# Performance work log

Hardware: AMD Instinct MI355X
Metric: run time of the kernel (lower is better)

The kernel has to match this reference:

```python
import jax, jax.numpy as jnp
import numpy as np

N_IN, N_LAT, LEN_T, N_SHIFT = 128, 21, 51, 50
N_HID, BATCH = 4, 2048


def identity_init(n_rows, n_cols):
    A = np.zeros((n_rows, n_cols), np.float32)
    if n_rows >= n_cols:
        k = n_rows - n_cols + 1
        for c in range(n_cols):
            A[c:c + k, c] = 1.0 / k
    else:
        k = n_cols - n_rows + 1
        for r in range(n_rows):
            A[r, r:r + k] = 1.0 / k
    return jnp.asarray(A)


def setup_inputs() -> dict:
    key = jax.random.key(0)
    ks = jax.random.split(key, 8)
    s = 0.05
    return {
        'inputs': jax.random.normal(ks[0], (BATCH, LEN_T, N_IN), dtype=jnp.float32),
        'enc_W': jax.random.normal(ks[1], (N_HID, N_IN, N_IN), dtype=jnp.float32) * s,
        'enc_b': jnp.zeros((N_HID, N_IN), jnp.float32),
        'enc_Wout': jax.random.normal(ks[2], (N_IN, N_IN), dtype=jnp.float32) * s,
        'enc_bout': jnp.zeros((N_IN,), jnp.float32),
        'dec_W': jax.random.normal(ks[3], (N_HID, N_IN, N_IN), dtype=jnp.float32) * s,
        'dec_b': jnp.zeros((N_HID, N_IN), jnp.float32),
        'dec_Wout': jax.random.normal(ks[4], (N_IN, N_IN), dtype=jnp.float32) * s,
        'dec_bout': jnp.zeros((N_IN,), jnp.float32),
        'W_enc_inner': identity_init(N_IN, N_LAT),
        'L': jnp.eye(N_LAT, dtype=jnp.float32),
        'W_dec_inner': identity_init(N_LAT, N_IN),
    }


def res_block(x, Ws, bs, Wout, bout):
    # DenseResBlock: ReLU hidden dense stack + linear output + identity skip
    h = x
    for i in range(Ws.shape[0]):
        h = jax.nn.relu(h @ Ws[i] + bs[i])
    return h @ Wout + bout + x


def reference(inputs, enc_W, enc_b, enc_Wout, enc_bout,
              dec_W, dec_b, dec_Wout, dec_bout,
              W_enc_inner, L, W_dec_inner):
    B = inputs.shape[0]
    len_pred = LEN_T - N_SHIFT  # = 1

    # ---- autoencoder branch (all timesteps flattened into rows) ----
    auto_in = inputs.reshape(-1, N_IN)                       # [B*T, n_in]
    part_enc = res_block(auto_in, enc_W, enc_b, enc_Wout, enc_bout)
    full_enc = part_enc @ W_enc_inner                        # [B*T, n_lat]
    part_dec = full_enc @ W_dec_inner                        # [B*T, n_in]
    autoencoder_output = res_block(part_dec, dec_W, dec_b, dec_Wout, dec_bout)
    autoencoder_output = autoencoder_output.reshape(B, LEN_T, N_IN)
    outer_auto_output = res_block(part_enc, dec_W, dec_b, dec_Wout, dec_bout)
    outer_auto_output = outer_auto_output.reshape(B, LEN_T, N_IN)

    # ---- prediction branch: recurrent application of Koopman operator L ----
    pred_in = inputs[:, :len_pred, :].reshape(-1, N_IN)      # [B*len_pred, n_in]
    cur = res_block(pred_in, enc_W, enc_b, enc_Wout, enc_bout) @ W_enc_inner

    def step(cur_enc, _):
        adv = cur_enc @ L                                    # [B*len_pred, n_lat]
        dec = res_block(adv @ W_dec_inner, dec_W, dec_b, dec_Wout, dec_bout)
        return adv, dec

    _, preds = jax.lax.scan(step, cur, None, length=N_SHIFT)  # [S, B*lp, n_in]
    preds = preds.reshape(N_SHIFT, B, len_pred, N_IN)
    predictions = preds.transpose(1, 0, 2, 3).reshape(B, N_SHIFT * len_pred, N_IN)

    return autoencoder_output, outer_auto_output, predictions
```

## Files before the change

kernel.cpp:

```cpp
#include <hip/hip_runtime.h>
#include <stdint.h>


typedef _Float16 h8 __attribute__((ext_vector_type(8)));
typedef _Float16 h4 __attribute__((ext_vector_type(4)));
typedef float    f4 __attribute__((ext_vector_type(4)));

#define ROWS_AUTO 104448
#define NT64      1632
#define NUNITS    1952

#define WT_ENCW      0
#define WT_ENCWOUT   (4*16384)
#define WT_DECW      (5*16384)
#define WT_DECWOUT   (9*16384)
#define WT_COMB      (10*16384)

#define MFULL_OFF_B 0x60000
#define ACH_OFF_B   0x200000
#define PE_OFF_B    0x220000
#define PET0_OFF_B  0x1C00000

#define H0 0
#define H1 16384
#define H2 32768
#define H3 49152
#define LDSE 51712
#define LDSD 68096

#define hsw(rl, c) ((rl)*256 + ((((c)) ^ ((rl) & 7)) << 4))

#define PIN(B) asm volatile("" : "+v"(B[0]), "+v"(B[1]), "+v"(B[2]), "+v"(B[3]), \
                                 "+v"(B[4]), "+v"(B[5]), "+v"(B[6]), "+v"(B[7]))

__device__ __forceinline__ f4 mfma16(h8 a, h8 b, f4 c) {
  return __builtin_amdgcn_mfma_f32_16x16x32_f16(a, b, c, 0, 0, 0);
}
__device__ __forceinline__ h8 cvt8(f4 a, f4 b) {
  h8 r;
  r[0]=(_Float16)a[0]; r[1]=(_Float16)a[1]; r[2]=(_Float16)a[2]; r[3]=(_Float16)a[3];
  r[4]=(_Float16)b[0]; r[5]=(_Float16)b[1]; r[6]=(_Float16)b[2]; r[7]=(_Float16)b[3];
  return r;
}
__device__ __forceinline__ void loadW(h8 B[8], const _Float16* gW, int nbase, int r15, int hi) {
#pragma unroll
  for (int nt = 0; nt < 2; ++nt)
#pragma unroll
    for (int ks = 0; ks < 4; ++ks)
      B[nt*4+ks] = *(const h8*)(gW + (size_t)(nbase + nt*16 + r15)*128 + ks*32 + hi*8);
}

__device__ __forceinline__ void mmF4s(const char* sm, int hb, const h8 B[8],
                                      f4 acc[4][2], int r15, int hi) {
#pragma unroll
  for (int rt = 0; rt < 4; ++rt) { acc[rt][0] = (f4){0,0,0,0}; acc[rt][1] = (f4){0,0,0,0}; }
#pragma unroll
  for (int ks = 0; ks < 4; ++ks) {
    int c = ks*4 + hi;
    h8 a[4];
#pragma unroll
    for (int rt = 0; rt < 4; ++rt) a[rt] = *(const h8*)(sm + hb + hsw(rt*16 + r15, c));
#pragma unroll
    for (int rt = 0; rt < 4; ++rt) {
      acc[rt][0] = mfma16(B[ks],   a[rt], acc[rt][0]);
      acc[rt][1] = mfma16(B[4+ks], a[rt], acc[rt][1]);
    }
  }
}

__device__ __forceinline__ void hw4s(char* sm, int hb, int wbase, const f4 acc[4][2],
                                     const float* bl, int bo, int r15, int hi) {
  f4 bb0 = *(const f4*)(bl + bo + wbase + hi*4);
  f4 bb1 = *(const f4*)(bl + bo + wbase + 16 + hi*4);
  int bo2 = (hi & 1) * 8;
#pragma unroll
  for (int nt = 0; nt < 2; ++nt) {
    int c = ((wbase + nt*16) >> 3) + (hi >> 1);
    f4 bb = nt ? bb1 : bb0;
#pragma unroll
    for (int rt = 0; rt < 4; ++rt) {
      int row = rt*16 + r15;
      h4 p;
#pragma unroll
      for (int d = 0; d < 4; ++d) p[d] = (_Float16)fmaxf(acc[rt][nt][d] + bb[d], 0.f);
      *(h4*)(sm + hb + row*256 + ((c ^ (row & 7)) << 4) + bo2) = p;
    }
  }
}
__device__ __forceinline__ void hw4r(char* sm, int hb, int wbase, const f4 acc[4][2],
                                     int r15, int hi) {
  int bo2 = (hi & 1) * 8;
#pragma unroll
  for (int nt = 0; nt < 2; ++nt) {
    int c = ((wbase + nt*16) >> 3) + (hi >> 1);
#pragma unroll
    for (int rt = 0; rt < 4; ++rt) {
      int row = rt*16 + r15;
      h4 p;
#pragma unroll
      for (int d = 0; d < 4; ++d) p[d] = (_Float16)acc[rt][nt][d];
      *(h4*)(sm + hb + row*256 + ((c ^ (row & 7)) << 4) + bo2) = p;
    }
  }
}

__device__ __forceinline__ void epi_store(char* sm, int hskip, int htr, int wbase,
                                          const f4 acc[4][2], const float* bl,
                                          float* dst, int rstride,
                                          int tid, int r15, int hi) {
  f4 bb0 = *(const f4*)(bl + 512 + wbase + hi*4);
  f4 bb1 = *(const f4*)(bl + 512 + wbase + 16 + hi*4);
  int bo2 = (hi & 1) * 8;
#pragma unroll
  for (int nt = 0; nt < 2; ++nt) {
    int c = ((wbase + nt*16) >> 3) + (hi >> 1);
    int q = (wbase >> 2) + nt*4 + hi;
    f4 bb = nt ? bb1 : bb0;
#pragma unroll
    for (int rt = 0; rt < 4; ++rt) {
      int row = rt*16 + r15;
      h4 sk = *(const h4*)(sm + hskip + row*256 + ((c ^ (row & 7)) << 4) + bo2);
      f4 v;
#pragma unroll
      for (int d = 0; d < 4; ++d) v[d] = acc[rt][nt][d] + bb[d] + (float)sk[d];
      *(f4*)(sm + htr + row*512 + ((q ^ ((row & 7) << 2)) << 4)) = v;
    }
  }
  __syncthreads();
#pragma unroll
  for (int i = 0; i < 8; ++i) {
    int idx = i*256 + tid, row = idx >> 5, q = idx & 31;
    f4 v = *(const f4*)(sm + htr + row*512 + ((q ^ ((row & 7) << 2)) << 4));
    *(f4*)(dst + (size_t)row*rstride + q*4) = v;
  }
}

#define LAYD(HIN, HOUT, BW, BO) do {                                 \
    mmF4s(sm, HIN, BW, acc, r15, hi);                                \
    hw4s(sm, HOUT, wbase, acc, bl, BO, r15, hi);                     \
    __syncthreads();                                                 \
  } while (0)


__global__ __launch_bounds__(512) void k_prep(
    const float* __restrict__ encW, const float* __restrict__ encWout,
    const float* __restrict__ decW, const float* __restrict__ decWout,
    const float* __restrict__ L,
    _Float16* __restrict__ wt, float* __restrict__ ach) {
  __shared__ float chA[441], chB[441];
  int m = blockIdx.y, tid = threadIdx.x;
  if (m == 10) {
    if (blockIdx.x != 0) return;
    if (tid < 441) chA[tid] = L[tid];
    __syncthreads();
    for (int s = 0; s < 50; ++s) {
      if (tid < 441) ach[s*441 + tid] = chA[tid];
      if (s == 49) break;
      if (tid < 441) {
        int i = tid / 21, j = tid % 21; float a = 0.f;
        for (int k = 0; k < 21; ++k) a += chA[i*21 + k] * L[k*21 + j];
        chB[tid] = a;
      }
      __syncthreads();
      if (tid < 441) chA[tid] = chB[tid];
      __syncthreads();
    }
    return;
  }
  int idx = blockIdx.x*512 + tid;
  if (idx >= 16384) return;
  const float* src; _Float16* dst;
  if (m < 4)       { src = encW + m*16384;     dst = wt + WT_ENCW + m*16384; }
  else if (m == 4) { src = encWout;            dst = wt + WT_ENCWOUT; }
  else if (m < 9)  { src = decW + (m-5)*16384; dst = wt + WT_DECW + (m-5)*16384; }
  else             { src = decWout;            dst = wt + WT_DECWOUT; }
  int n = idx >> 7, k = idx & 127;
  dst[idx] = (_Float16)src[k*128 + n];
}

__global__ __launch_bounds__(512) void k_aux(
    const float* __restrict__ ach, const float* __restrict__ wencI,
    const float* __restrict__ wdecI,
    _Float16* __restrict__ mfull, _Float16* __restrict__ wt) {
  __shared__ float T1[2688];
  __shared__ float sa[441];
  int s = blockIdx.x, t = threadIdx.x;
  if (s < 50) {
    if (t < 441) sa[t] = ach[s*441 + t];
    __syncthreads();
    for (int idx = t; idx < 2688; idx += 512) {
      int k = idx / 21, j = idx % 21;
      float a = 0.f;
      for (int u = 0; u < 21; ++u) a += wencI[k*21 + u] * sa[u*21 + j];
      T1[idx] = a;
    }
  } else {
    for (int idx = t; idx < 2688; idx += 512) T1[idx] = wencI[idx];
  }
  __syncthreads();
  _Float16* dst = (s < 50) ? (mfull + (size_t)s*16384) : (wt + WT_COMB);
  for (int idx = t; idx < 16384; idx += 512) {
    int n = idx >> 7, k = idx & 127;
    float a = 0.f;
    for (int j = 0; j < 21; ++j) a += T1[k*21 + j] * wdecI[j*128 + n];
    dst[idx] = (_Float16)a;
  }
}


__global__ __launch_bounds__(256, 2) void k_enc(
    const float* __restrict__ x, const _Float16* __restrict__ wt,
    const float* __restrict__ enc_b, const float* __restrict__ enc_bout,
    _Float16* __restrict__ pe_ws, _Float16* __restrict__ pet0) {
  __shared__ char sm[LDSE];
  float* bl = (float*)(sm + 49152);
  int tid = threadIdx.x, lane = tid & 63;
  int r15 = lane & 15, hi = lane >> 4;
  int wbase = (tid >> 6) * 32;
  h8 B0[8], B1[8], B2[8], B3[8], B4[8];
  loadW(B0, wt + WT_ENCW,           wbase, r15, hi);
  loadW(B1, wt + WT_ENCW + 16384,   wbase, r15, hi);
  loadW(B2, wt + WT_ENCW + 2*16384, wbase, r15, hi);
  loadW(B3, wt + WT_ENCW + 3*16384, wbase, r15, hi);
  loadW(B4, wt + WT_ENCWOUT,        wbase, r15, hi);
  PIN(B0); PIN(B1); PIN(B2); PIN(B3); PIN(B4);
  bl[tid] = enc_b[tid]; bl[256 + tid] = enc_b[256 + tid];
  if (tid < 128) bl[512 + tid] = enc_bout[tid];
  f4 acc[4][2];

  for (int t = blockIdx.x; t < NT64; t += gridDim.x) {
    size_t rb = (size_t)t * 64;
#pragma unroll
    for (int i = 0; i < 4; ++i) {
      int idx = i*256 + tid, rl = idx >> 4, c = idx & 15;
      const float* s = x + (rb + rl)*128 + c*8;
      f4 v0 = *(const f4*)s, v1 = *(const f4*)(s + 4);
      *(h8*)(sm + H0 + hsw(rl, c)) = cvt8(v0, v1);
    }
    __syncthreads();
    LAYD(H0, H1, B0, 0); LAYD(H1, H2, B1, 128);
    LAYD(H2, H1, B2, 256); LAYD(H1, H2, B3, 384);
    mmF4s(sm, H2, B4, acc, r15, hi);
    {
      f4 bb0 = *(const f4*)(bl + 512 + wbase + hi*4);
      f4 bb1 = *(const f4*)(bl + 512 + wbase + 16 + hi*4);
      int bo2 = (hi & 1) * 8;
#pragma unroll
      for (int nt = 0; nt < 2; ++nt) {
        int c = ((wbase + nt*16) >> 3) + (hi >> 1);
        f4 bb = nt ? bb1 : bb0;
#pragma unroll
        for (int rt = 0; rt < 4; ++rt) {
          int row = rt*16 + r15;
          int soff = row*256 + ((c ^ (row & 7)) << 4) + bo2;
          h4 sk = *(const h4*)(sm + H0 + soff);
          h4 p;
#pragma unroll
          for (int d = 0; d < 4; ++d) p[d] = (_Float16)(acc[rt][nt][d] + bb[d] + (float)sk[d]);
          *(h4*)(sm + H1 + soff) = p;
        }
      }
    }
    __syncthreads();
    {
      char* g = (char*)(pe_ws) + (size_t)t*16384;
#pragma unroll
      for (int i = 0; i < 4; ++i) {
        int idx = i*256 + tid, off = idx*16;
        f4 v = *(const f4*)(sm + H1 + off);
        *(f4*)(g + off) = v;
        int rl = idx >> 4, slot = idx & 15;
        size_t rg = rb + (size_t)rl;
        if (rg % 51u == 0u) {
          int c = slot ^ (rl & 7);
          *(f4*)((char*)pet0 + (rg/51u)*256 + c*16) = v;
        }
      }
    }
  }
}


__global__ __launch_bounds__(256, 2) void k_decpred(
    const _Float16* __restrict__ wt, const _Float16* __restrict__ pe_ws,
    const _Float16* __restrict__ pet0, const _Float16* __restrict__ mfull,
    const float* __restrict__ dec_b, const float* __restrict__ dec_bout,
    float* __restrict__ out1, float* __restrict__ out2, float* __restrict__ out3) {
  __shared__ char sm[LDSD];
  float* bl = (float*)(sm + 65536);
  int tid = threadIdx.x, lane = tid & 63;
  int r15 = lane & 15, hi = lane >> 4;
  int wbase = (tid >> 6) * 32;
  h8 B0[8], B1[8], B2[8], B3[8], B4[8];
  loadW(B0, wt + WT_DECW,           wbase, r15, hi);
  loadW(B1, wt + WT_DECW + 16384,   wbase, r15, hi);
  loadW(B2, wt + WT_DECW + 2*16384, wbase, r15, hi);
  loadW(B3, wt + WT_DECW + 3*16384, wbase, r15, hi);
  loadW(B4, wt + WT_DECWOUT,        wbase, r15, hi);
  PIN(B0); PIN(B1); PIN(B2); PIN(B3); PIN(B4);
  bl[tid] = dec_b[tid]; bl[256 + tid] = dec_b[256 + tid];
  if (tid < 128) bl[512 + tid] = dec_bout[tid];
  f4 acc[4][2];

  for (int u = blockIdx.x; u < NUNITS; u += gridDim.x) {
    __syncthreads();
    if (u < NT64) {
      const char* src = (const char*)pe_ws + (size_t)u*16384;
      float* d2 = out2 + (size_t)u*64*128;
      float* d1 = out1 + (size_t)u*64*128;
#pragma unroll
      for (int i = 0; i < 4; ++i) {
        int off = (i*256 + tid)*16;
        *(f4*)(sm + H0 + off) = *(const f4*)(src + off);
      }
      __syncthreads();
      LAYD(H0, H1, B0, 0); LAYD(H1, H2, B1, 128);
      LAYD(H2, H1, B2, 256); LAYD(H1, H2, B3, 384);
      mmF4s(sm, H2, B4, acc, r15, hi);
      __syncthreads();
      epi_store(sm, H0, H1, wbase, acc, bl, d2, 128, tid, r15, hi);
      {
        h8 Bc[8];
        loadW(Bc, wt + WT_COMB, wbase, r15, hi);
        mmF4s(sm, H0, Bc, acc, r15, hi);
      }
      hw4r(sm, H3, wbase, acc, r15, hi);
      __syncthreads();
      LAYD(H3, H0, B0, 0); LAYD(H0, H1, B1, 128);
      LAYD(H1, H0, B2, 256); LAYD(H0, H1, B3, 384);
      mmF4s(sm, H1, B4, acc, r15, hi);
      __syncthreads();
      epi_store(sm, H3, H0, wbase, acc, bl, d1, 128, tid, r15, hi);
    } else {
      int p = u - NT64, rtile = p / 10, chunk = p % 10;
#pragma unroll
      for (int i = 0; i < 4; ++i) {
        int idx = i*256 + tid, rl = idx >> 4, c = idx & 15;
        f4 v = *(const f4*)((const char*)pet0 + (size_t)(rtile*64 + rl)*256 + c*16);
        *(f4*)(sm + H0 + hsw(rl, c)) = v;
      }
      __syncthreads();
      for (int s = chunk*5; s < chunk*5 + 5; ++s) {
        {
          h8 Bm[8];
          loadW(Bm, mfull + (size_t)s*16384, wbase, r15, hi);
          mmF4s(sm, H0, Bm, acc, r15, hi);
        }
        hw4r(sm, H1, wbase, acc, r15, hi);
        __syncthreads();
        LAYD(H1, H2, B0, 0); LAYD(H2, H3, B1, 128);
        LAYD(H3, H2, B2, 256); LAYD(H2, H3, B3, 384);
        mmF4s(sm, H3, B4, acc, r15, hi);
        __syncthreads();
        epi_store(sm, H1, H2, wbase, acc, bl,
                  out3 + ((size_t)rtile*64*50 + s)*128, 50*128, tid, r15, hi);
        __syncthreads();
      }
    }
  }
}


extern "C" void kernel_launch(void* const* d_in, const int* in_sizes, int n_in,
                              void* d_out, int out_size, void* d_ws, size_t ws_size,
                              hipStream_t stream) {
  const float* x        = (const float*)d_in[0];
  const float* encW     = (const float*)d_in[1];
  const float* enc_b    = (const float*)d_in[2];
  const float* encWout  = (const float*)d_in[3];
  const float* enc_bout = (const float*)d_in[4];
  const float* decW     = (const float*)d_in[5];
  const float* dec_b    = (const float*)d_in[6];
  const float* decWout  = (const float*)d_in[7];
  const float* dec_bout = (const float*)d_in[8];
  const float* wencI    = (const float*)d_in[9];
  const float* L        = (const float*)d_in[10];
  const float* wdecI    = (const float*)d_in[11];

  char* ws = (char*)d_ws;
  _Float16* wt    = (_Float16*)ws;
  _Float16* mfull = (_Float16*)(ws + MFULL_OFF_B);
  float*    ach   = (float*)(ws + ACH_OFF_B);
  _Float16* pe_ws = (_Float16*)(ws + PE_OFF_B);
  _Float16* pet0  = (_Float16*)(ws + PET0_OFF_B);

  float* out1 = (float*)d_out;
  float* out2 = out1 + (size_t)ROWS_AUTO*128;
  float* out3 = out2 + (size_t)ROWS_AUTO*128;

  hipLaunchKernelGGL(k_prep, dim3(32, 11), dim3(512), 0, stream,
                     encW, encWout, decW, decWout, L, wt, ach);
  hipLaunchKernelGGL(k_aux, dim3(51), dim3(512), 0, stream,
                     ach, wencI, wdecI, mfull, wt);
  hipLaunchKernelGGL(k_enc, dim3(512), dim3(256), 0, stream,
                     x, wt, enc_b, enc_bout, pe_ws, pet0);
  hipLaunchKernelGGL(k_decpred, dim3(512), dim3(256), 0, stream,
                     wt, pe_ws, pet0, mfull, dec_b, dec_bout, out1, out2, out3);
}
```

Before: 224.6 us.

## Fuse encoder and decoder passes into one kernel with streamed double-buffered weights

Merges the encoder and autoencoder-decoder passes into a single kernel, so the encoded fp16 tiles stay in LDS and the pe_ws round trip through global memory goes away. Instead of pinning all five weight matrices in registers, each layer's weights are prefetched from global/L2 into a second register buffer while the current layer computes. This lowers register pressure and allows three blocks per CU. The prediction branch moves to its own kernel with a fixed grid of 800 blocks doing two steps each, and biases are stored in LDS as fp16. The trade-off is repeated weight loads on every layer from L2 and slightly lower bias precision.

```diff
diff --git a/kernel.cpp b/kernel.cpp
--- a/kernel.cpp
+++ b/kernel.cpp
@@ -8,7 +8,6 @@
 
 #define ROWS_AUTO 104448
 #define NT64      1632
-#define NUNITS    1952
 
 #define WT_ENCW      0
 #define WT_ENCWOUT   (4*16384)
@@ -18,15 +17,18 @@
 
 #define MFULL_OFF_B 0x60000
 #define ACH_OFF_B   0x200000
-#define PE_OFF_B    0x220000
-#define PET0_OFF_B  0x1C00000
-
-#define H0 0
-#define H1 16384
-#define H2 32768
-#define H3 49152
-#define LDSE 51712
-#define LDSD 68096
+#define PET0_OFF_B  0x220000
+
+#define LA 0
+#define LB 16384
+#define LC 32768
+#define LDSM (49152 + 2560)
+#define LDSP (49152 + 1280)
+
+#define ENC_B  0
+#define ENC_BO 512
+#define DEC_B  640
+#define DEC_BO 1152
 
 #define hsw(rl, c) ((rl)*256 + ((((c)) ^ ((rl) & 7)) << 4))
 
@@ -69,25 +71,25 @@
 }
 
 __device__ __forceinline__ void hw4s(char* sm, int hb, int wbase, const f4 acc[4][2],
-                                     const float* bl, int bo, int r15, int hi) {
-  f4 bb0 = *(const f4*)(bl + bo + wbase + hi*4);
-  f4 bb1 = *(const f4*)(bl + bo + wbase + 16 + hi*4);
+                                     const _Float16* blh, int bo, int r15, int hi) {
+  h4 b0 = *(const h4*)(blh + bo + wbase + hi*4);
+  h4 b1 = *(const h4*)(blh + bo + wbase + 16 + hi*4);
   int bo2 = (hi & 1) * 8;
 #pragma unroll
   for (int nt = 0; nt < 2; ++nt) {
     int c = ((wbase + nt*16) >> 3) + (hi >> 1);
-    f4 bb = nt ? bb1 : bb0;
+    h4 bb = nt ? b1 : b0;
 #pragma unroll
     for (int rt = 0; rt < 4; ++rt) {
       int row = rt*16 + r15;
       h4 p;
 #pragma unroll
-      for (int d = 0; d < 4; ++d) p[d] = (_Float16)fmaxf(acc[rt][nt][d] + bb[d], 0.f);
+      for (int d = 0; d < 4; ++d) p[d] = (_Float16)fmaxf(acc[rt][nt][d] + (float)bb[d], 0.f);
       *(h4*)(sm + hb + row*256 + ((c ^ (row & 7)) << 4) + bo2) = p;
     }
   }
 }
-__device__ __forceinline__ void hw4r(char* sm, int hb, int wbase, const f4 acc[4][2],
+__device__ __forceinline__ void hw4r(char* sm, int hb, int wbase, const h4 pr[4][2],
                                      int r15, int hi) {
   int bo2 = (hi & 1) * 8;
 #pragma unroll
@@ -96,49 +98,49 @@
 #pragma unroll
     for (int rt = 0; rt < 4; ++rt) {
       int row = rt*16 + r15;
-      h4 p;
-#pragma unroll
-      for (int d = 0; d < 4; ++d) p[d] = (_Float16)acc[rt][nt][d];
-      *(h4*)(sm + hb + row*256 + ((c ^ (row & 7)) << 4) + bo2) = p;
-    }
-  }
-}
-
-__device__ __forceinline__ void epi_store(char* sm, int hskip, int htr, int wbase,
-                                          const f4 acc[4][2], const float* bl,
-                                          float* dst, int rstride,
-                                          int tid, int r15, int hi) {
-  f4 bb0 = *(const f4*)(bl + 512 + wbase + hi*4);
-  f4 bb1 = *(const f4*)(bl + 512 + wbase + 16 + hi*4);
+      *(h4*)(sm + hb + row*256 + ((c ^ (row & 7)) << 4) + bo2) = pr[rt][nt];
+    }
+  }
+}
+
+template<int SKIP>
+__device__ __forceinline__ void epi_store(char* sm, int hskip, const h4 pr[4][2], int wbase,
+                                          const f4 acc[4][2], const _Float16* blh, int bout,
+                                          float* dst, int rstride, int tid, int r15, int hi) {
+  h4 b0 = *(const h4*)(blh + bout + wbase + hi*4);
+  h4 b1 = *(const h4*)(blh + bout + wbase + 16 + hi*4);
   int bo2 = (hi & 1) * 8;
 #pragma unroll
   for (int nt = 0; nt < 2; ++nt) {
     int c = ((wbase + nt*16) >> 3) + (hi >> 1);
     int q = (wbase >> 2) + nt*4 + hi;
-    f4 bb = nt ? bb1 : bb0;
+    h4 bb = nt ? b1 : b0;
 #pragma unroll
     for (int rt = 0; rt < 4; ++rt) {
       int row = rt*16 + r15;
-      h4 sk = *(const h4*)(sm + hskip + row*256 + ((c ^ (row & 7)) << 4) + bo2);
+      h4 sk = SKIP ? pr[rt][nt]
+                   : *(const h4*)(sm + hskip + row*256 + ((c ^ (row & 7)) << 4) + bo2);
       f4 v;
 #pragma unroll
-      for (int d = 0; d < 4; ++d) v[d] = acc[rt][nt][d] + bb[d] + (float)sk[d];
-      *(f4*)(sm + htr + row*512 + ((q ^ ((row & 7) << 2)) << 4)) = v;
+      for (int d = 0; d < 4; ++d) v[d] = acc[rt][nt][d] + (float)bb[d] + (float)sk[d];
+      *(f4*)(sm + LB + row*512 + ((q ^ ((row & 7) << 2)) << 4)) = v;
     }
   }
   __syncthreads();
 #pragma unroll
   for (int i = 0; i < 8; ++i) {
     int idx = i*256 + tid, row = idx >> 5, q = idx & 31;
-    f4 v = *(const f4*)(sm + htr + row*512 + ((q ^ ((row & 7) << 2)) << 4));
+    f4 v = *(const f4*)(sm + LB + row*512 + ((q ^ ((row & 7) << 2)) << 4));
     *(f4*)(dst + (size_t)row*rstride + q*4) = v;
   }
 }
 
-#define LAYD(HIN, HOUT, BW, BO) do {                                 \
-    mmF4s(sm, HIN, BW, acc, r15, hi);                                \
-    hw4s(sm, HOUT, wbase, acc, bl, BO, r15, hi);                     \
-    __syncthreads();                                                 \
+#define PHASE(LIN, LOUT, BC, BN, NXT, BO) do {            \
+    loadW(BN, NXT, wbase, r15, hi);                        \
+    mmF4s(sm, LIN, BC, acc, r15, hi);                      \
+    hw4s(sm, LOUT, wbase, acc, blh, BO, r15, hi);          \
+    PIN(BN);                                               \
+    __syncthreads();                                       \
   } while (0)
 
 
@@ -208,25 +210,29 @@
 }
 
 
-__global__ __launch_bounds__(256, 2) void k_enc(
+__global__ __launch_bounds__(256, 3) void k_main(
     const float* __restrict__ x, const _Float16* __restrict__ wt,
     const float* __restrict__ enc_b, const float* __restrict__ enc_bout,
-    _Float16* __restrict__ pe_ws, _Float16* __restrict__ pet0) {
-  __shared__ char sm[LDSE];
-  float* bl = (float*)(sm + 49152);
+    const float* __restrict__ dec_b, const float* __restrict__ dec_bout,
+    float* __restrict__ out1, float* __restrict__ out2, _Float16* __restrict__ pet0) {
+  __shared__ char sm[LDSM];
+  _Float16* blh = (_Float16*)(sm + 49152);
   int tid = threadIdx.x, lane = tid & 63;
   int r15 = lane & 15, hi = lane >> 4;
   int wbase = (tid >> 6) * 32;
-  h8 B0[8], B1[8], B2[8], B3[8], B4[8];
-  loadW(B0, wt + WT_ENCW,           wbase, r15, hi);
-  loadW(B1, wt + WT_ENCW + 16384,   wbase, r15, hi);
-  loadW(B2, wt + WT_ENCW + 2*16384, wbase, r15, hi);
-  loadW(B3, wt + WT_ENCW + 3*16384, wbase, r15, hi);
-  loadW(B4, wt + WT_ENCWOUT,        wbase, r15, hi);
-  PIN(B0); PIN(B1); PIN(B2); PIN(B3); PIN(B4);
-  bl[tid] = enc_b[tid]; bl[256 + tid] = enc_b[256 + tid];
-  if (tid < 128) bl[512 + tid] = enc_bout[tid];
+  h8 Ba[8], Bb[8];
   f4 acc[4][2];
+  h4 pd[4][2];
+
+  for (int i = tid; i < 1280; i += 256) {
+    float v;
+    if (i < 512) v = enc_b[i];
+    else if (i < 640) v = enc_bout[i - 512];
+    else if (i < 1152) v = dec_b[i - 640];
+    else v = dec_bout[i - 1152];
+    blh[i] = (_Float16)v;
+  }
+  loadW(Ba, wt + WT_ENCW, wbase, r15, hi);
 
   for (int t = blockIdx.x; t < NT64; t += gridDim.x) {
     size_t rb = (size_t)t * 64;
@@ -235,128 +241,140 @@
       int idx = i*256 + tid, rl = idx >> 4, c = idx & 15;
       const float* s = x + (rb + rl)*128 + c*8;
       f4 v0 = *(const f4*)s, v1 = *(const f4*)(s + 4);
-      *(h8*)(sm + H0 + hsw(rl, c)) = cvt8(v0, v1);
-    }
-    __syncthreads();
-    LAYD(H0, H1, B0, 0); LAYD(H1, H2, B1, 128);
-    LAYD(H2, H1, B2, 256); LAYD(H1, H2, B3, 384);
-    mmF4s(sm, H2, B4, acc, r15, hi);
+      *(h8*)(sm + LA + hsw(rl, c)) = cvt8(v0, v1);
+    }
+    PIN(Ba);
+    __syncthreads();
+    PHASE(LA, LB, Ba, Bb, wt + WT_ENCW + 16384,   ENC_B + 0);
+    PHASE(LB, LC, Bb, Ba, wt + WT_ENCW + 2*16384, ENC_B + 128);
+    PHASE(LC, LB, Ba, Bb, wt + WT_ENCW + 3*16384, ENC_B + 256);
+    PHASE(LB, LC, Bb, Ba, wt + WT_ENCWOUT,        ENC_B + 384);
+    loadW(Bb, wt + WT_COMB, wbase, r15, hi);
+    mmF4s(sm, LC, Ba, acc, r15, hi);
     {
-      f4 bb0 = *(const f4*)(bl + 512 + wbase + hi*4);
-      f4 bb1 = *(const f4*)(bl + 512 + wbase + 16 + hi*4);
+      h4 b0 = *(const h4*)(blh + ENC_BO + wbase + hi*4);
+      h4 b1 = *(const h4*)(blh + ENC_BO + wbase + 16 + hi*4);
       int bo2 = (hi & 1) * 8;
 #pragma unroll
       for (int nt = 0; nt < 2; ++nt) {
         int c = ((wbase + nt*16) >> 3) + (hi >> 1);
-        f4 bb = nt ? bb1 : bb0;
+        h4 bb = nt ? b1 : b0;
 #pragma unroll
         for (int rt = 0; rt < 4; ++rt) {
           int row = rt*16 + r15;
-          int soff = row*256 + ((c ^ (row & 7)) << 4) + bo2;
-          h4 sk = *(const h4*)(sm + H0 + soff);
+          int soff = LA + row*256 + ((c ^ (row & 7)) << 4) + bo2;
+          h4 sk = *(const h4*)(sm + soff);
           h4 p;
 #pragma unroll
-          for (int d = 0; d < 4; ++d) p[d] = (_Float16)(acc[rt][nt][d] + bb[d] + (float)sk[d]);
-          *(h4*)(sm + H1 + soff) = p;
+          for (int d = 0; d < 4; ++d) p[d] = (_Float16)(acc[rt][nt][d] + (float)bb[d] + (float)sk[d]);
+          *(h4*)(sm + soff) = p;
         }
       }
     }
+    PIN(Bb);
     __syncthreads();
     {
-      char* g = (char*)(pe_ws) + (size_t)t*16384;
 #pragma unroll
       for (int i = 0; i < 4; ++i) {
-        int idx = i*256 + tid, off = idx*16;
-        f4 v = *(const f4*)(sm + H1 + off);
-        *(f4*)(g + off) = v;
-        int rl = idx >> 4, slot = idx & 15;
+        int idx = i*256 + tid, rl = idx >> 4, slot = idx & 15;
         size_t rg = rb + (size_t)rl;
         if (rg % 51u == 0u) {
           int c = slot ^ (rl & 7);
-          *(f4*)((char*)pet0 + (rg/51u)*256 + c*16) = v;
+          *(f4*)((char*)pet0 + (rg/51u)*256 + c*16) = *(const f4*)(sm + LA + idx*16);
         }
       }
     }
-  }
-}
-
-
-__global__ __launch_bounds__(256, 2) void k_decpred(
-    const _Float16* __restrict__ wt, const _Float16* __restrict__ pe_ws,
-    const _Float16* __restrict__ pet0, const _Float16* __restrict__ mfull,
+    loadW(Ba, wt + WT_DECW, wbase, r15, hi);
+    mmF4s(sm, LA, Bb, acc, r15, hi);
+#pragma unroll
+    for (int rt = 0; rt < 4; ++rt)
+#pragma unroll
+      for (int nt = 0; nt < 2; ++nt)
+#pragma unroll
+        for (int d = 0; d < 4; ++d) pd[rt][nt][d] = (_Float16)acc[rt][nt][d];
+    PHASE(LA, LB, Ba, Bb, wt + WT_DECW + 16384,   DEC_B + 0);
+    PHASE(LB, LC, Bb, Ba, wt + WT_DECW + 2*16384, DEC_B + 128);
+    PHASE(LC, LB, Ba, Bb, wt + WT_DECW + 3*16384, DEC_B + 256);
+    PHASE(LB, LC, Bb, Ba, wt + WT_DECWOUT,        DEC_B + 384);
+    loadW(Bb, wt + WT_DECW, wbase, r15, hi);
+    mmF4s(sm, LC, Ba, acc, r15, hi);
+    PIN(Bb);
+    __syncthreads();
+    epi_store<0>(sm, LA, pd, wbase, acc, blh, DEC_BO,
+                 out2 + rb*128, 128, tid, r15, hi);
+    hw4r(sm, LA, wbase, pd, r15, hi);
+    __syncthreads();
+    PHASE(LA, LB, Bb, Ba, wt + WT_DECW + 16384,   DEC_B + 0);
+    PHASE(LB, LC, Ba, Bb, wt + WT_DECW + 2*16384, DEC_B + 128);
+    PHASE(LC, LB, Bb, Ba, wt + WT_DECW + 3*16384, DEC_B + 256);
+    PHASE(LB, LC, Ba, Bb, wt + WT_DECWOUT,        DEC_B + 384);
+    loadW(Ba, wt + WT_ENCW, wbase, r15, hi);
+    mmF4s(sm, LC, Bb, acc, r15, hi);
+    PIN(Ba);
+    __syncthreads();
+    epi_store<1>(sm, 0, pd, wbase, acc, blh, DEC_BO,
+                 out1 + rb*128, 128, tid, r15, hi);
+    __syncthreads();
+  }
+}
+
+
+__global__ __launch_bounds__(256, 3) void k_pred(
+    const _Float16* __restrict__ pet0, const _Float16* __restrict__ wt,
+    const _Float16* __restrict__ mfull,
     const float* __restrict__ dec_b, const float* __restrict__ dec_bout,
-    float* __restrict__ out1, float* __restrict__ out2, float* __restrict__ out3) {
-  __shared__ char sm[LDSD];
-  float* bl = (float*)(sm + 65536);
+    float* __restrict__ out3) {
+  __shared__ char sm[LDSP];
+  _Float16* blh = (_Float16*)(sm + 49152);
   int tid = threadIdx.x, lane = tid & 63;
   int r15 = lane & 15, hi = lane >> 4;
   int wbase = (tid >> 6) * 32;
-  h8 B0[8], B1[8], B2[8], B3[8], B4[8];
-  loadW(B0, wt + WT_DECW,           wbase, r15, hi);
-  loadW(B1, wt + WT_DECW + 16384,   wbase, r15, hi);
-  loadW(B2, wt + WT_DECW + 2*16384, wbase, r15, hi);
-  loadW(B3, wt + WT_DECW + 3*16384, wbase, r15, hi);
-  loadW(B4, wt + WT_DECWOUT,        wbase, r15, hi);
-  PIN(B0); PIN(B1); PIN(B2); PIN(B3); PIN(B4);
-  bl[tid] = dec_b[tid]; bl[256 + tid] = dec_b[256 + tid];
-  if (tid < 128) bl[512 + tid] = dec_bout[tid];
+  h8 Ba[8], Bb[8];
   f4 acc[4][2];
-
-  for (int u = blockIdx.x; u < NUNITS; u += gridDim.x) {
-    __syncthreads();
-    if (u < NT64) {
-      const char* src = (const char*)pe_ws + (size_t)u*16384;
-      float* d2 = out2 + (size_t)u*64*128;
-      float* d1 = out1 + (size_t)u*64*128;
-#pragma unroll
-      for (int i = 0; i < 4; ++i) {
-        int off = (i*256 + tid)*16;
-        *(f4*)(sm + H0 + off) = *(const f4*)(src + off);
-      }
-      __syncthreads();
-      LAYD(H0, H1, B0, 0); LAYD(H1, H2, B1, 128);
-      LAYD(H2, H1, B2, 256); LAYD(H1, H2, B3, 384);
-      mmF4s(sm, H2, B4, acc, r15, hi);
-      __syncthreads();
-      epi_store(sm, H0, H1, wbase, acc, bl, d2, 128, tid, r15, hi);
-      {
-        h8 Bc[8];
-        loadW(Bc, wt + WT_COMB, wbase, r15, hi);
-        mmF4s(sm, H0, Bc, acc, r15, hi);
-      }
-      hw4r(sm, H3, wbase, acc, r15, hi);
-      __syncthreads();
-      LAYD(H3, H0, B0, 0); LAYD(H0, H1, B1, 128);
-      LAYD(H1, H0, B2, 256); LAYD(H0, H1, B3, 384);
-      mmF4s(sm, H1, B4, acc, r15, hi);
-      __syncthreads();
-      epi_store(sm, H3, H0, wbase, acc, bl, d1, 128, tid, r15, hi);
-    } else {
-      int p = u - NT64, rtile = p / 10, chunk = p % 10;
-#pragma unroll
-      for (int i = 0; i < 4; ++i) {
-        int idx = i*256 + tid, rl = idx >> 4, c = idx & 15;
-        f4 v = *(const f4*)((const char*)pet0 + (size_t)(rtile*64 + rl)*256 + c*16);
-        *(f4*)(sm + H0 + hsw(rl, c)) = v;
-      }
-      __syncthreads();
-      for (int s = chunk*5; s < chunk*5 + 5; ++s) {
-        {
-          h8 Bm[8];
-          loadW(Bm, mfull + (size_t)s*16384, wbase, r15, hi);
-          mmF4s(sm, H0, Bm, acc, r15, hi);
-        }
-        hw4r(sm, H1, wbase, acc, r15, hi);
-        __syncthreads();
-        LAYD(H1, H2, B0, 0); LAYD(H2, H3, B1, 128);
-        LAYD(H3, H2, B2, 256); LAYD(H2, H3, B3, 384);
-        mmF4s(sm, H3, B4, acc, r15, hi);
-        __syncthreads();
-        epi_store(sm, H1, H2, wbase, acc, bl,
-                  out3 + ((size_t)rtile*64*50 + s)*128, 50*128, tid, r15, hi);
-        __syncthreads();
-      }
-    }
+  h4 di[4][2];
+
+  for (int i = tid; i < 640; i += 256)
+    blh[i] = (_Float16)(i < 512 ? dec_b[i] : dec_bout[i - 512]);
+
+  int rtile = blockIdx.x / 25;
+  int chunk = blockIdx.x % 25;
+  int s0 = chunk * 2;
+  loadW(Ba, mfull + (size_t)s0*16384, wbase, r15, hi);
+#pragma unroll
+  for (int i = 0; i < 4; ++i) {
+    int idx = i*256 + tid, rl = idx >> 4, c = idx & 15;
+    f4 v = *(const f4*)((const char*)pet0 + (size_t)(rtile*64 + rl)*256 + c*16);
+    *(f4*)(sm + LA + hsw(rl, c)) = v;
+  }
+  PIN(Ba);
+  __syncthreads();
+
+  for (int s = s0; s < s0 + 2; ++s) {
+    loadW(Bb, wt + WT_DECW, wbase, r15, hi);
+    mmF4s(sm, LA, Ba, acc, r15, hi);
+#pragma unroll
+    for (int rt = 0; rt < 4; ++rt)
+#pragma unroll
+      for (int nt = 0; nt < 2; ++nt)
+#pragma unroll
+        for (int d = 0; d < 4; ++d) di[rt][nt][d] = (_Float16)acc[rt][nt][d];
+    hw4r(sm, LB, wbase, di, r15, hi);
+    PIN(Bb);
+    __syncthreads();
+    PHASE(LB, LC, Bb, Ba, wt + WT_DECW + 16384,   0);
+    PHASE(LC, LB, Ba, Bb, wt + WT_DECW + 2*16384, 128);
+    PHASE(LB, LC, Bb, Ba, wt + WT_DECW + 3*16384, 256);
+    PHASE(LC, LB, Ba, Bb, wt + WT_DECWOUT,        384);
+    {
+      int sn = (s + 1 < 50) ? s + 1 : 49;
+      loadW(Ba, mfull + (size_t)sn*16384, wbase, r15, hi);
+    }
+    mmF4s(sm, LB, Bb, acc, r15, hi);
+    PIN(Ba);
+    __syncthreads();
+    epi_store<1>(sm, 0, di, wbase, acc, blh, 512,
+                 out3 + ((size_t)rtile*64*50 + s)*128, 50*128, tid, r15, hi);
+    __syncthreads();
   }
 }
 
@@ -381,7 +399,6 @@
   _Float16* wt    = (_Float16*)ws;
   _Float16* mfull = (_Float16*)(ws + MFULL_OFF_B);
   float*    ach   = (float*)(ws + ACH_OFF_B);
-  _Float16* pe_ws = (_Float16*)(ws + PE_OFF_B);
   _Float16* pet0  = (_Float16*)(ws + PET0_OFF_B);
 
   float* out1 = (float*)d_out;
@@ -392,8 +409,8 @@
                      encW, encWout, decW, decWout, L, wt, ach);
   hipLaunchKernelGGL(k_aux, dim3(51), dim3(512), 0, stream,
                      ach, wencI, wdecI, mfull, wt);
-  hipLaunchKernelGGL(k_enc, dim3(512), dim3(256), 0, stream,
-                     x, wt, enc_b, enc_bout, pe_ws, pet0);
-  hipLaunchKernelGGL(k_decpred, dim3(512), dim3(256), 0, stream,
-                     wt, pe_ws, pet0, mfull, dec_b, dec_bout, out1, out2, out3);
-}
+  hipLaunchKernelGGL(k_main, dim3(768), dim3(256), 0, stream,
+                     x, wt, enc_b, enc_bout, dec_b, dec_bout, out1, out2, pet0);
+  hipLaunchKernelGGL(k_pred, dim3(800), dim3(256), 0, stream,
+                     pet0, wt, mfull, dec_b, dec_bout, out3);
+}
```

Measured after the change: 337.8 us. 1.5x slower.

## Split 128 output columns across 8 waves with 512-thread blocks

Applied to the files above, without the earlier changes.

Blocks go from 256 to 512 threads, and each wave now computes 16 output columns instead of 32. That halves the per-wave register-resident weight fragments and MFMA accumulators, so more waves fit per CU (launch bounds 512,4). Biases are stored in LDS as fp16 to shrink the footprint. The prediction work units are split finer (25 chunks of 2 steps instead of 10 of 5) to balance load, and k_enc writes its encoder output back in place. In exchange there are more threads per barrier and more repeated A-fragment LDS reads per column, and storing biases as fp16 slightly lowers precision.

```diff
diff --git a/kernel.cpp b/kernel.cpp
--- a/kernel.cpp
+++ b/kernel.cpp
@@ -8,7 +8,7 @@
 
 #define ROWS_AUTO 104448
 #define NT64      1632
-#define NUNITS    1952
+#define NUNITS    2432
 
 #define WT_ENCW      0
 #define WT_ENCWOUT   (4*16384)
@@ -25,13 +25,12 @@
 #define H1 16384
 #define H2 32768
 #define H3 49152
-#define LDSE 51712
-#define LDSD 68096
+#define LDSE (49152 + 1280)
+#define LDSD (65536 + 1280)
 
 #define hsw(rl, c) ((rl)*256 + ((((c)) ^ ((rl) & 7)) << 4))
 
-#define PIN(B) asm volatile("" : "+v"(B[0]), "+v"(B[1]), "+v"(B[2]), "+v"(B[3]), \
-                                 "+v"(B[4]), "+v"(B[5]), "+v"(B[6]), "+v"(B[7]))
+#define PIN4(B) asm volatile("" : "+v"(B[0]), "+v"(B[1]), "+v"(B[2]), "+v"(B[3]))
 
 __device__ __forceinline__ f4 mfma16(h8 a, h8 b, f4 c) {
   return __builtin_amdgcn_mfma_f32_16x16x32_f16(a, b, c, 0, 0, 0);
@@ -42,103 +41,81 @@
   r[4]=(_Float16)b[0]; r[5]=(_Float16)b[1]; r[6]=(_Float16)b[2]; r[7]=(_Float16)b[3];
   return r;
 }
-__device__ __forceinline__ void loadW(h8 B[8], const _Float16* gW, int nbase, int r15, int hi) {
-#pragma unroll
-  for (int nt = 0; nt < 2; ++nt)
-#pragma unroll
-    for (int ks = 0; ks < 4; ++ks)
-      B[nt*4+ks] = *(const h8*)(gW + (size_t)(nbase + nt*16 + r15)*128 + ks*32 + hi*8);
-}
-
-__device__ __forceinline__ void mmF4s(const char* sm, int hb, const h8 B[8],
-                                      f4 acc[4][2], int r15, int hi) {
-#pragma unroll
-  for (int rt = 0; rt < 4; ++rt) { acc[rt][0] = (f4){0,0,0,0}; acc[rt][1] = (f4){0,0,0,0}; }
+__device__ __forceinline__ void loadW16(h8 B[4], const _Float16* gW, int wbase, int r15, int hi) {
+#pragma unroll
+  for (int ks = 0; ks < 4; ++ks)
+    B[ks] = *(const h8*)(gW + (size_t)(wbase + r15)*128 + ks*32 + hi*8);
+}
+
+__device__ __forceinline__ void mm16(const char* sm, int hb, const h8 B[4],
+                                     f4 acc[4], int r15, int hi) {
+#pragma unroll
+  for (int rt = 0; rt < 4; ++rt) acc[rt] = (f4){0,0,0,0};
 #pragma unroll
   for (int ks = 0; ks < 4; ++ks) {
     int c = ks*4 + hi;
-    h8 a[4];
-#pragma unroll
-    for (int rt = 0; rt < 4; ++rt) a[rt] = *(const h8*)(sm + hb + hsw(rt*16 + r15, c));
 #pragma unroll
     for (int rt = 0; rt < 4; ++rt) {
-      acc[rt][0] = mfma16(B[ks],   a[rt], acc[rt][0]);
-      acc[rt][1] = mfma16(B[4+ks], a[rt], acc[rt][1]);
-    }
-  }
-}
-
-__device__ __forceinline__ void hw4s(char* sm, int hb, int wbase, const f4 acc[4][2],
-                                     const float* bl, int bo, int r15, int hi) {
-  f4 bb0 = *(const f4*)(bl + bo + wbase + hi*4);
-  f4 bb1 = *(const f4*)(bl + bo + wbase + 16 + hi*4);
-  int bo2 = (hi & 1) * 8;
-#pragma unroll
-  for (int nt = 0; nt < 2; ++nt) {
-    int c = ((wbase + nt*16) >> 3) + (hi >> 1);
-    f4 bb = nt ? bb1 : bb0;
-#pragma unroll
-    for (int rt = 0; rt < 4; ++rt) {
-      int row = rt*16 + r15;
-      h4 p;
-#pragma unroll
-      for (int d = 0; d < 4; ++d) p[d] = (_Float16)fmaxf(acc[rt][nt][d] + bb[d], 0.f);
-      *(h4*)(sm + hb + row*256 + ((c ^ (row & 7)) << 4) + bo2) = p;
-    }
-  }
-}
-__device__ __forceinline__ void hw4r(char* sm, int hb, int wbase, const f4 acc[4][2],
-                                     int r15, int hi) {
-  int bo2 = (hi & 1) * 8;
-#pragma unroll
-  for (int nt = 0; nt < 2; ++nt) {
-    int c = ((wbase + nt*16) >> 3) + (hi >> 1);
-#pragma unroll
-    for (int rt = 0; rt < 4; ++rt) {
-      int row = rt*16 + r15;
-      h4 p;
-#pragma unroll
-      for (int d = 0; d < 4; ++d) p[d] = (_Float16)acc[rt][nt][d];
-      *(h4*)(sm + hb + row*256 + ((c ^ (row & 7)) << 4) + bo2) = p;
-    }
-  }
-}
-
-__device__ __forceinline__ void epi_store(char* sm, int hskip, int htr, int wbase,
-                                          const f4 acc[4][2], const float* bl,
-                                          float* dst, int rstride,
-                                          int tid, int r15, int hi) {
-  f4 bb0 = *(const f4*)(bl + 512 + wbase + hi*4);
-  f4 bb1 = *(const f4*)(bl + 512 + wbase + 16 + hi*4);
-  int bo2 = (hi & 1) * 8;
-#pragma unroll
-  for (int nt = 0; nt < 2; ++nt) {
-    int c = ((wbase + nt*16) >> 3) + (hi >> 1);
-    int q = (wbase >> 2) + nt*4 + hi;
-    f4 bb = nt ? bb1 : bb0;
-#pragma unroll
-    for (int rt = 0; rt < 4; ++rt) {
-      int row = rt*16 + r15;
-      h4 sk = *(const h4*)(sm + hskip + row*256 + ((c ^ (row & 7)) << 4) + bo2);
-      f4 v;
-#pragma unroll
-      for (int d = 0; d < 4; ++d) v[d] = acc[rt][nt][d] + bb[d] + (float)sk[d];
-      *(f4*)(sm + htr + row*512 + ((q ^ ((row & 7) << 2)) << 4)) = v;
-    }
+      h8 a = *(const h8*)(sm + hb + hsw(rt*16 + r15, c));
+      acc[rt] = mfma16(B[ks], a, acc[rt]);
+    }
+  }
+}
+
+__device__ __forceinline__ void hw16s(char* sm, int hb, int wbase, const f4 acc[4],
+                                      const _Float16* blh, int bo, int r15, int hi) {
+  h4 bb = *(const h4*)(blh + bo + wbase + hi*4);
+  int c = (wbase >> 3) + (hi >> 1), bo2 = (hi & 1) * 8;
+#pragma unroll
+  for (int rt = 0; rt < 4; ++rt) {
+    int row = rt*16 + r15;
+    h4 p;
+#pragma unroll
+    for (int d = 0; d < 4; ++d) p[d] = (_Float16)fmaxf(acc[rt][d] + (float)bb[d], 0.f);
+    *(h4*)(sm + hb + row*256 + ((c ^ (row & 7)) << 4) + bo2) = p;
+  }
+}
+__device__ __forceinline__ void hw16a(char* sm, int hb, int wbase, const f4 acc[4],
+                                      int r15, int hi) {
+  int c = (wbase >> 3) + (hi >> 1), bo2 = (hi & 1) * 8;
+#pragma unroll
+  for (int rt = 0; rt < 4; ++rt) {
+    int row = rt*16 + r15;
+    h4 p;
+#pragma unroll
+    for (int d = 0; d < 4; ++d) p[d] = (_Float16)acc[rt][d];
+    *(h4*)(sm + hb + row*256 + ((c ^ (row & 7)) << 4) + bo2) = p;
+  }
+}
+
+__device__ __forceinline__ void epi16(char* sm, int hskip, int trb, int wbase,
+                                      const f4 acc[4], const _Float16* blh, int bout,
+                                      float* dst, int rstride, int tid, int r15, int hi) {
+  h4 bb = *(const h4*)(blh + bout + wbase + hi*4);
+  int c = (wbase >> 3) + (hi >> 1), bo2 = (hi & 1) * 8;
+  int q = (wbase >> 2) + hi;
+#pragma unroll
+  for (int rt = 0; rt < 4; ++rt) {
+    int row = rt*16 + r15;
+    h4 sk = *(const h4*)(sm + hskip + row*256 + ((c ^ (row & 7)) << 4) + bo2);
+    f4 v;
+#pragma unroll
+    for (int d = 0; d < 4; ++d) v[d] = acc[rt][d] + (float)bb[d] + (float)sk[d];
+    *(f4*)(sm + trb + row*512 + ((q ^ ((row & 7) << 2)) << 4)) = v;
   }
   __syncthreads();
 #pragma unroll
-  for (int i = 0; i < 8; ++i) {
-    int idx = i*256 + tid, row = idx >> 5, q = idx & 31;
-    f4 v = *(const f4*)(sm + htr + row*512 + ((q ^ ((row & 7) << 2)) << 4));
-    *(f4*)(dst + (size_t)row*rstride + q*4) = v;
-  }
-}
-
-#define LAYD(HIN, HOUT, BW, BO) do {                                 \
-    mmF4s(sm, HIN, BW, acc, r15, hi);                                \
-    hw4s(sm, HOUT, wbase, acc, bl, BO, r15, hi);                     \
-    __syncthreads();                                                 \
+  for (int i = 0; i < 4; ++i) {
+    int idx = i*512 + tid, row = idx >> 5, qq = idx & 31;
+    f4 v = *(const f4*)(sm + trb + row*512 + ((qq ^ ((row & 7) << 2)) << 4));
+    *(f4*)(dst + (size_t)row*rstride + qq*4) = v;
+  }
+}
+
+#define LAY(LIN, LOUT, BW, BO) do {                        \
+    mm16(sm, LIN, BW, acc, r15, hi);                       \
+    hw16s(sm, LOUT, wbase, acc, blh, BO, r15, hi);         \
+    __syncthreads();                                       \
   } while (0)
 
 
@@ -208,66 +185,60 @@
 }
 
 
-__global__ __launch_bounds__(256, 2) void k_enc(
+__global__ __launch_bounds__(512, 4) void k_enc(
     const float* __restrict__ x, const _Float16* __restrict__ wt,
     const float* __restrict__ enc_b, const float* __restrict__ enc_bout,
     _Float16* __restrict__ pe_ws, _Float16* __restrict__ pet0) {
   __shared__ char sm[LDSE];
-  float* bl = (float*)(sm + 49152);
+  _Float16* blh = (_Float16*)(sm + 49152);
   int tid = threadIdx.x, lane = tid & 63;
   int r15 = lane & 15, hi = lane >> 4;
-  int wbase = (tid >> 6) * 32;
-  h8 B0[8], B1[8], B2[8], B3[8], B4[8];
-  loadW(B0, wt + WT_ENCW,           wbase, r15, hi);
-  loadW(B1, wt + WT_ENCW + 16384,   wbase, r15, hi);
-  loadW(B2, wt + WT_ENCW + 2*16384, wbase, r15, hi);
-  loadW(B3, wt + WT_ENCW + 3*16384, wbase, r15, hi);
-  loadW(B4, wt + WT_ENCWOUT,        wbase, r15, hi);
-  PIN(B0); PIN(B1); PIN(B2); PIN(B3); PIN(B4);
-  bl[tid] = enc_b[tid]; bl[256 + tid] = enc_b[256 + tid];
-  if (tid < 128) bl[512 + tid] = enc_bout[tid];
-  f4 acc[4][2];
+  int wbase = (tid >> 6) * 16;
+  h8 B0[4], B1[4], B2[4], B3[4], B4[4];
+  loadW16(B0, wt + WT_ENCW,           wbase, r15, hi);
+  loadW16(B1, wt + WT_ENCW + 16384,   wbase, r15, hi);
+  loadW16(B2, wt + WT_ENCW + 2*16384, wbase, r15, hi);
+  loadW16(B3, wt + WT_ENCW + 3*16384, wbase, r15, hi);
+  loadW16(B4, wt + WT_ENCWOUT,        wbase, r15, hi);
+  PIN4(B0); PIN4(B1); PIN4(B2); PIN4(B3); PIN4(B4);
+  for (int i = tid; i < 640; i += 512)
+    blh[i] = (_Float16)(i < 512 ? enc_b[i] : enc_bout[i - 512]);
+  f4 acc[4];
 
   for (int t = blockIdx.x; t < NT64; t += gridDim.x) {
     size_t rb = (size_t)t * 64;
 #pragma unroll
-    for (int i = 0; i < 4; ++i) {
-      int idx = i*256 + tid, rl = idx >> 4, c = idx & 15;
+    for (int i = 0; i < 2; ++i) {
+      int idx = i*512 + tid, rl = idx >> 4, c = idx & 15;
       const float* s = x + (rb + rl)*128 + c*8;
       f4 v0 = *(const f4*)s, v1 = *(const f4*)(s + 4);
       *(h8*)(sm + H0 + hsw(rl, c)) = cvt8(v0, v1);
     }
     __syncthreads();
-    LAYD(H0, H1, B0, 0); LAYD(H1, H2, B1, 128);
-    LAYD(H2, H1, B2, 256); LAYD(H1, H2, B3, 384);
-    mmF4s(sm, H2, B4, acc, r15, hi);
+    LAY(H0, H1, B0, 0); LAY(H1, H2, B1, 128);
+    LAY(H2, H1, B2, 256); LAY(H1, H2, B3, 384);
+    mm16(sm, H2, B4, acc, r15, hi);
     {
-      f4 bb0 = *(const f4*)(bl + 512 + wbase + hi*4);
-      f4 bb1 = *(const f4*)(bl + 512 + wbase + 16 + hi*4);
-      int bo2 = (hi & 1) * 8;
-#pragma unroll
-      for (int nt = 0; nt < 2; ++nt) {
-        int c = ((wbase + nt*16) >> 3) + (hi >> 1);
-        f4 bb = nt ? bb1 : bb0;
-#pragma unroll
-        for (int rt = 0; rt < 4; ++rt) {
-          int row = rt*16 + r15;
-          int soff = row*256 + ((c ^ (row & 7)) << 4) + bo2;
-          h4 sk = *(const h4*)(sm + H0 + soff);
-          h4 p;
-#pragma unroll
-          for (int d = 0; d < 4; ++d) p[d] = (_Float16)(acc[rt][nt][d] + bb[d] + (float)sk[d]);
-          *(h4*)(sm + H1 + soff) = p;
-        }
+      h4 bb = *(const h4*)(blh + 512 + wbase + hi*4);
+      int c = (wbase >> 3) + (hi >> 1), bo2 = (hi & 1) * 8;
+#pragma unroll
+      for (int rt = 0; rt < 4; ++rt) {
+        int row = rt*16 + r15;
+        int soff = H0 + row*256 + ((c ^ (row & 7)) << 4) + bo2;
+        h4 sk = *(const h4*)(sm + soff);
+        h4 p;
+#pragma unroll
+        for (int d = 0; d < 4; ++d) p[d] = (_Float16)(acc[rt][d] + (float)bb[d] + (float)sk[d]);
+        *(h4*)(sm + soff) = p;
       }
     }
     __syncthreads();
     {
       char* g = (char*)(pe_ws) + (size_t)t*16384;
 #pragma unroll
-      for (int i = 0; i < 4; ++i) {
-        int idx = i*256 + tid, off = idx*16;
-        f4 v = *(const f4*)(sm + H1 + off);
+      for (int i = 0; i < 2; ++i) {
+        int idx = i*512 + tid, off = idx*16;
+        f4 v = *(const f4*)(sm + H0 + off);
         *(f4*)(g + off) = v;
         int rl = idx >> 4, slot = idx & 15;
         size_t rg = rb + (size_t)rl;
@@ -277,83 +248,84 @@
         }
       }
     }
-  }
-}
-
-
-__global__ __launch_bounds__(256, 2) void k_decpred(
+    __syncthreads();
+  }
+}
+
+
+__global__ __launch_bounds__(512, 4) void k_decpred(
     const _Float16* __restrict__ wt, const _Float16* __restrict__ pe_ws,
     const _Float16* __restrict__ pet0, const _Float16* __restrict__ mfull,
     const float* __restrict__ dec_b, const float* __restrict__ dec_bout,
     float* __restrict__ out1, float* __restrict__ out2, float* __restrict__ out3) {
   __shared__ char sm[LDSD];
-  float* bl = (float*)(sm + 65536);
+  _Float16* blh = (_Float16*)(sm + 65536);
   int tid = threadIdx.x, lane = tid & 63;
   int r15 = lane & 15, hi = lane >> 4;
-  int wbase = (tid >> 6) * 32;
-  h8 B0[8], B1[8], B2[8], B3[8], B4[8];
-  loadW(B0, wt + WT_DECW,           wbase, r15, hi);
-  loadW(B1, wt + WT_DECW + 16384,   wbase, r15, hi);
-  loadW(B2, wt + WT_DECW + 2*16384, wbase, r15, hi);
-  loadW(B3, wt + WT_DECW + 3*16384, wbase, r15, hi);
-  loadW(B4, wt + WT_DECWOUT,        wbase, r15, hi);
-  PIN(B0); PIN(B1); PIN(B2); PIN(B3); PIN(B4);
-  bl[tid] = dec_b[tid]; bl[256 + tid] = dec_b[256 + tid];
-  if (tid < 128) bl[512 + tid] = dec_bout[tid];
-  f4 acc[4][2];
+  int wbase = (tid >> 6) * 16;
+  h8 B0[4], B1[4], B2[4], B3[4], B4[4];
+  loadW16(B0, wt + WT_DECW,           wbase, r15, hi);
+  loadW16(B1, wt + WT_DECW + 16384,   wbase, r15, hi);
+  loadW16(B2, wt + WT_DECW + 2*16384, wbase, r15, hi);
+  loadW16(B3, wt + WT_DECW + 3*16384, wbase, r15, hi);
+  loadW16(B4, wt + WT_DECWOUT,        wbase, r15, hi);
+  PIN4(B0); PIN4(B1); PIN4(B2); PIN4(B3); PIN4(B4);
+  for (int i = tid; i < 640; i += 512)
+    blh[i] = (_Float16)(i < 512 ? dec_b[i] : dec_bout[i - 512]);
+  f4 acc[4];
 
   for (int u = blockIdx.x; u < NUNITS; u += gridDim.x) {
     __syncthreads();
     if (u < NT64) {
       const char* src = (const char*)pe_ws + (size_t)u*16384;
-      float* d2 = out2 + (size_t)u*64*128;
-      float* d1 = out1 + (size_t)u*64*128;
-#pragma unroll
-      for (int i = 0; i < 4; ++i) {
-        int off = (i*256 + tid)*16;
+#pragma unroll
+      for (int i = 0; i < 2; ++i) {
+        int off = (i*512 + tid)*16;
         *(f4*)(sm + H0 + off) = *(const f4*)(src + off);
       }
       __syncthreads();
-      LAYD(H0, H1, B0, 0); LAYD(H1, H2, B1, 128);
-      LAYD(H2, H1, B2, 256); LAYD(H1, H2, B3, 384);
-      mmF4s(sm, H2, B4, acc, r15, hi);
-      __syncthreads();
-      epi_store(sm, H0, H1, wbase, acc, bl, d2, 128, tid, r15, hi);
+      LAY(H0, H1, B0, 0); LAY(H1, H2, B1, 128);
+      LAY(H2, H1, B2, 256); LAY(H1, H2, B3, 384);
+      mm16(sm, H2, B4, acc, r15, hi);
+      __syncthreads();
+      epi16(sm, H0, H1, wbase, acc, blh, 512,
+            out2 + (size_t)u*64*128, 128, tid, r15, hi);
       {
-        h8 Bc[8];
-        loadW(Bc, wt + WT_COMB, wbase, r15, hi);
-        mmF4s(sm, H0, Bc, acc, r15, hi);
-      }
-      hw4r(sm, H3, wbase, acc, r15, hi);
-      __syncthreads();
-      LAYD(H3, H0, B0, 0); LAYD(H0, H1, B1, 128);
-      LAYD(H1, H0, B2, 256); LAYD(H0, H1, B3, 384);
-      mmF4s(sm, H1, B4, acc, r15, hi);
-      __syncthreads();
-      epi_store(sm, H3, H0, wbase, acc, bl, d1, 128, tid, r15, hi);
+        h8 Bc[4];
+        loadW16(Bc, wt + WT_COMB, wbase, r15, hi);
+        mm16(sm, H0, Bc, acc, r15, hi);
+      }
+      hw16a(sm, H3, wbase, acc, r15, hi);
+      __syncthreads();
+      LAY(H3, H0, B0, 0); LAY(H0, H2, B1, 128);
+      LAY(H2, H0, B2, 256); LAY(H0, H2, B3, 384);
+      mm16(sm, H2, B4, acc, r15, hi);
+      __syncthreads();
+      epi16(sm, H3, H1, wbase, acc, blh, 512,
+            out1 + (size_t)u*64*128, 128, tid, r15, hi);
     } else {
-      int p = u - NT64, rtile = p / 10, chunk = p % 10;
-#pragma unroll
-      for (int i = 0; i < 4; ++i) {
-        int idx = i*256 + tid, rl = idx >> 4, c = idx & 15;
+      int p = u - NT64, rtile = p / 25, chunk = p % 25;
+#pragma unroll
+      for (int i = 0; i < 2; ++i) {
+        int idx = i*512 + tid, rl = idx >> 4, c = idx & 15;
         f4 v = *(const f4*)((const char*)pet0 + (size_t)(rtile*64 + rl)*256 + c*16);
         *(f4*)(sm + H0 + hsw(rl, c)) = v;
       }
       __syncthreads();
-      for (int s = chunk*5; s < chunk*5 + 5; ++s) {
+      for (int s = chunk*2; s < chunk*2 + 2; ++s) {
         {
-          h8 Bm[8];
-          loadW(Bm, mfull + (size_t)s*16384, wbase, r15, hi);
-          mmF4s(sm, H0, Bm, acc, r15, hi);
+          h8 Bm[4];
+          loadW16(Bm, mfull + (size_t)s*16384, wbase, r15, hi);
+          mm16(sm, H0, Bm, acc, r15, hi);
         }
-        hw4r(sm, H1, wbase, acc, r15, hi);
+        hw16a(sm, H1, wbase, acc, r15, hi);
         __syncthreads();
-        LAYD(H1, H2, B0, 0); LAYD(H2, H3, B1, 128);
-        LAYD(H3, H2, B2, 256); LAYD(H2, H3, B3, 384);
-        mmF4s(sm, H3, B4, acc, r15, hi);
+        LAY(H1, H2, B0, 0); LAY(H2, H3, B1, 128);
+        LAY(H3, H2, B2, 256); LAY(H2, H3, B3, 384);
+        mm16(sm, H3, B4, acc, r15, hi);
         __syncthreads();
-        epi_store(sm, H1, H2, wbase, acc, bl,
-                  out3 + ((size_t)rtile*64*50 + s)*128, 50*128, tid, r15, hi);
+        epi16(sm, H1, H2, wbase, acc, blh, 512,
+              out3 + ((size_t)rtile*64*50 + s)*128, 50*128, tid, r15, hi);
         __syncthreads();
       }
     }
@@ -392,8 +364,8 @@
                      encW, encWout, decW, decWout, L, wt, ach);
   hipLaunchKernelGGL(k_aux, dim3(51), dim3(512), 0, stream,
                      ach, wencI, wdecI, mfull, wt);
-  hipLaunchKernelGGL(k_enc, dim3(512), dim3(256), 0, stream,
+  hipLaunchKernelGGL(k_enc, dim3(512), dim3(512), 0, stream,
                      x, wt, enc_b, enc_bout, pe_ws, pet0);
-  hipLaunchKernelGGL(k_decpred, dim3(512), dim3(256), 0, stream,
+  hipLaunchKernelGGL(k_decpred, dim3(512), dim3(512), 0, stream,
                      wt, pe_ws, pet0, mfull, dec_b, dec_bout, out1, out2, out3);
 }
```

After: 225.5 us. About the same (+0.4%).
